# Performance work log

Measured on AMD Instinct MI355X. Metric: run time of the kernel, lower is better.

## Reference

```python
import jax, jax.numpy as jnp
import numpy as np

NUM_HEADS = 16
NEG_INF = -1e9


def setup_inputs() -> dict:
    key = jax.random.key(0)
    ks = jax.random.split(key, 12)
    T, B, E = 2048, 4, 1024
    s = 0.02
    inp = {
        "query": jax.random.normal(ks[0], (T, B, E), jnp.float32),
        "key": jax.random.normal(ks[1], (T, B, E), jnp.float32),
        "value": jax.random.normal(ks[2], (T, B, E), jnp.float32),
        # causal additive mask [T, S]: 0 on/below diagonal, -1e9 above
        "attn_mask": jnp.where(
            jnp.arange(T)[:, None] >= jnp.arange(T)[None, :], 0.0, NEG_INF
        ).astype(jnp.float32),
        "wq": jax.random.normal(ks[3], (E, E), jnp.float32) * s,
        "bq": jax.random.normal(ks[4], (E,), jnp.float32) * s,
        "wk": jax.random.normal(ks[5], (E, E), jnp.float32) * s,
        "bk": jax.random.normal(ks[6], (E,), jnp.float32) * s,
        "wv": jax.random.normal(ks[7], (E, E), jnp.float32) * s,
        "bv": jax.random.normal(ks[8], (E,), jnp.float32) * s,
        "wo": jax.random.normal(ks[9], (E, E), jnp.float32) * s,
        "bo": jax.random.normal(ks[10], (E,), jnp.float32) * s,
    }
    return inp


def reference(query, key, value, attn_mask, wq, bq, wk, bk, wv, bv, wo, bo):
    T, B, E = query.shape
    H = NUM_HEADS
    D = E // H
    scaling = D ** (-0.5)
    # projections (torch Linear: x @ W.T + b)
    q = (query @ wq.T + bq) * scaling          # [T, B, E]
    k = key @ wk.T + bk                         # [S, B, E]
    v = value @ wv.T + bv                       # [S, B, E]
    # -> [B*H, len, D]
    q = q.reshape(T, B * H, D).transpose(1, 0, 2)
    k = k.reshape(-1, B * H, D).transpose(1, 0, 2)
    v = v.reshape(-1, B * H, D).transpose(1, 0, 2)
    # scores [B*H, T, S], additive mask, softmax (dropout = identity in eval)
    attn_weights = jnp.einsum('ntd,nsd->nts', q, k) + attn_mask
    attn_weights = jax.nn.softmax(attn_weights, axis=-1)
    attn = jnp.einsum('nts,nsd->ntd', attn_weights, v)   # [B*H, T, D]
    attn = attn.transpose(1, 0, 2).reshape(T, B, E)
    return attn @ wo.T + bo
```

## Files before the change

### kernel.cpp

```cpp
#include <hip/hip_runtime.h>
#include <hip/hip_bf16.h>

typedef __hip_bfloat16 bf16;
typedef __attribute__((ext_vector_type(8))) short short8;
typedef __attribute__((ext_vector_type(4))) float float4v;
typedef __attribute__((ext_vector_type(2))) unsigned long long ull2;
typedef __attribute__((ext_vector_type(2))) unsigned int uint2v;

#define TLEN  2048
#define BATCH 4
#define EMB   1024
#define HEADS 16
#define HD    64
#define MROWS (TLEN*BATCH)
#define PSTRIDE 72
#define SMAX2 5.770780f
#define QSCALE 0.18033688f

#if __has_builtin(__builtin_amdgcn_exp2f)
#define EXP2(x) __builtin_amdgcn_exp2f(x)
#else
#define EXP2(x) exp2f(x)
#endif

__device__ __forceinline__ unsigned cvt_pk_bf16(float lo, float hi) {
    unsigned r;
    asm("v_cvt_pk_bf16_f32 %0, %1, %2" : "=v"(r) : "v"(lo), "v"(hi));
    return r;
}

__device__ __forceinline__ void gl2lds16(const bf16* g, bf16* l) {
    __builtin_amdgcn_global_load_lds(
        (const __attribute__((address_space(1))) void*)g,
        (__attribute__((address_space(3))) void*)l, 16, 0, 0);
}

__device__ __forceinline__ void store_out(float* p, float v)  { *p = v; }
__device__ __forceinline__ void store_out(bf16* p, float v)   { *p = __float2bfloat16(v); }

__device__ __forceinline__ void cvt8(const float* __restrict__ src,
                                     bf16* __restrict__ dst, int t) {
    const float4v a = ((const float4v*)src)[2*t];
    const float4v b = ((const float4v*)src)[2*t + 1];
    union { short8 v; bf16 h[8]; } u;
    u.h[0] = __float2bfloat16(a[0]);
    u.h[1] = __float2bfloat16(a[1]);
    u.h[2] = __float2bfloat16(a[2]);
    u.h[3] = __float2bfloat16(a[3]);
    u.h[4] = __float2bfloat16(b[0]);
    u.h[5] = __float2bfloat16(b[1]);
    u.h[6] = __float2bfloat16(b[2]);
    u.h[7] = __float2bfloat16(b[3]);
    ((short8*)dst)[t] = u.v;
}

__global__ __launch_bounds__(256)
void cvt_w(const float* __restrict__ wq, const float* __restrict__ wk,
           const float* __restrict__ wv, const float* __restrict__ wo,
           bf16* __restrict__ wqb, bf16* __restrict__ wkb,
           bf16* __restrict__ wvb, bf16* __restrict__ wob)
{
    const int id = blockIdx.x * 256 + threadIdx.x;
    const int NW = 1 << 17;
    const int w = id >> 17, off = id & (NW - 1);
    const float* s = w == 0 ? wq : (w == 1 ? wk : (w == 2 ? wv : wo));
    bf16*        d = w == 0 ? wqb : (w == 1 ? wkb : (w == 2 ? wvb : wob));
    cvt8(s, d, off);
}

template<int AMODE, typename OutT>
__device__ __forceinline__ void gemm_body(
    const void* __restrict__ Avp, const bf16* __restrict__ Bw,
    const float* __restrict__ bias, OutT* __restrict__ out,
    float scale, int mode, int bm, int bn)
{
    __shared__ __align__(16) bf16 smem[128*64*2];
    bf16* As = smem;
    bf16* Bs = smem + 128*64;
    const int tid  = threadIdx.x;
    const int lane = tid & 63;
    const int wave = tid >> 6;
    const int wm   = (wave >> 1) * 64;
    const int wn   = (wave & 1) * 64;
    const int quad = lane >> 4;
    const int l16  = lane & 15;
    const int hl   = wn >> 6;

    const int srow = tid >> 3;
    const int skc  = (tid & 7) ^ (srow & 7);
    const bf16*  Ag = nullptr;
    const float* Af = nullptr;
    if constexpr (AMODE == 0)
        Ag = (const bf16*)Avp + (size_t)(bm*128 + srow)*EMB + skc*8;
    else
        Af = (const float*)Avp + (size_t)(bm*128 + srow)*EMB + skc*8;
    const bf16* Bg = Bw + (size_t)(bn*128 + srow)*EMB + skc*8;
    bf16* Al = As + tid*8;
    bf16* Bl = Bs + tid*8;

    float4v acc[4][4];
    #pragma unroll
    for (int i=0;i<4;i++)
        #pragma unroll
        for (int j=0;j<4;j++) acc[i][j] = (float4v){0.f,0.f,0.f,0.f};

    for (int k0 = 0; k0 < EMB; k0 += 64) {
        float4v a0[4], a1[4];
        if constexpr (AMODE == 1) {
            #pragma unroll
            for (int g=0; g<4; g++) {
                const float* ap = Af + (size_t)g*32*EMB + k0;
                a0[g] = *(const float4v*)ap;
                a1[g] = *(const float4v*)(ap + 4);
            }
        }
        __syncthreads();
        #pragma unroll
        for (int g=0; g<4; g++)
            gl2lds16(Bg + (size_t)g*32*EMB + k0, Bl + g*2048);
        if constexpr (AMODE == 0) {
            #pragma unroll
            for (int g=0; g<4; g++)
                gl2lds16(Ag + (size_t)g*32*EMB + k0, Al + g*2048);
        } else {
            #pragma unroll
            for (int g=0; g<4; g++) {
                union { short8 v; unsigned u[4]; } p;
                p.u[0] = cvt_pk_bf16(a0[g][0], a0[g][1]);
                p.u[1] = cvt_pk_bf16(a0[g][2], a0[g][3]);
                p.u[2] = cvt_pk_bf16(a1[g][0], a1[g][1]);
                p.u[3] = cvt_pk_bf16(a1[g][2], a1[g][3]);
                *(short8*)(Al + g*2048) = p.v;
            }
        }
        __syncthreads();

        #pragma unroll
        for (int half=0; half<2; half++) {
            const int pc = (((half<<2) | quad) ^ (l16 & 7)) * 8;
            short8 af[4], bfr[4];
            #pragma unroll
            for (int i=0;i<4;i++)
                af[i] = *(const short8*)(As + (wm + i*16 + l16)*64 + pc);
            #pragma unroll
            for (int j=0;j<4;j++)
                bfr[j] = *(const short8*)(Bs + (wn + j*16 + l16)*64 + pc);
            #pragma unroll
            for (int i=0;i<4;i++)
                #pragma unroll
                for (int j=0;j<4;j++)
                    acc[i][j] = __builtin_amdgcn_mfma_f32_16x16x32_bf16(
                                    af[i], bfr[j], acc[i][j], 0, 0, 0);
        }
    }

    if (mode != 2) {
        #pragma unroll
        for (int i=0;i<4;i++) {
            #pragma unroll
            for (int j=0;j<4;j++) {
                const int n = bn*128 + wn + j*16 + l16;
                const float bf = bias[n];
                #pragma unroll
                for (int r=0;r<4;r++) {
                    const int m = bm*128 + wm + i*16 + quad*4 + r;
                    const float v = (acc[i][j][r] + bf) * scale;
                    size_t idx;
                    if (mode == 0) {
                        idx = (size_t)m*EMB + n;
                    } else {
                        const int t = m >> 2, b = m & 3;
                        const int h = n >> 6, d = n & 63;
                        idx = (((size_t)(b*HEADS + h))*TLEN + t)*HD + d;
                    }
                    store_out(out + idx, v);
                }
            }
        }
    } else {
        __syncthreads();
        bf16* Tb = smem;
        #pragma unroll
        for (int i=0;i<4;i++) {
            const int tc = (wm >> 4) + i;
            #pragma unroll
            for (int j=0;j<4;j++) {
                const int d = j*16 + l16;
                const float bf = bias[bn*128 + wn + d];
                #pragma unroll
                for (int r=0;r<4;r++) {
                    const float v = acc[i][j][r] + bf;
                    Tb[((((r<<1)|hl)*64 + d) << 5) + ((tc ^ (d & 7)) << 2) + quad]
                        = __float2bfloat16(v);
                }
            }
        }
        __syncthreads();
        bf16* ob = (bf16*)out;
        #pragma unroll
        for (int pass=0; pass<8; pass++) {
            const int row = pass*64 + (tid >> 2);
            const int c16 = tid & 3;
            const int b2  = row >> 7;
            const int h2l = (row >> 6) & 1;
            const int d   = row & 63;
            const int e   = d & 7;
            const unsigned long long lo =
                *(const unsigned long long*)(Tb + (row << 5) + ((( (2*c16)   ^ e) << 2)));
            const unsigned long long hi =
                *(const unsigned long long*)(Tb + (row << 5) + ((( (2*c16+1) ^ e) << 2)));
            ull2 val; val.x = lo; val.y = hi;
            *(ull2*)(ob + ((size_t)((b2*HEADS + bn*2 + h2l)*HD + d))*TLEN
                        + bm*32 + c16*8) = val;
        }
    }
}

__global__ __launch_bounds__(256, 2)
void gemm_qkv(const float* __restrict__ xq, const float* __restrict__ xk,
              const float* __restrict__ xv,
              const bf16* __restrict__ wq, const bf16* __restrict__ wk,
              const bf16* __restrict__ wv,
              const float* __restrict__ bq, const float* __restrict__ bk,
              const float* __restrict__ bv,
              bf16* __restrict__ oq, bf16* __restrict__ ok,
              bf16* __restrict__ ov)
{
    const int id  = blockIdx.x;
    const int xcd = id & 7;
    const int r   = id >> 3;
    const int z   = r >> 6;
    const int rem = r & 63;
    const int bm  = xcd + 8*(rem >> 3);
    const int bn  = rem & 7;

    const float* A  = z == 0 ? xq : (z == 1 ? xk : xv);
    const bf16*  W  = z == 0 ? wq : (z == 1 ? wk : wv);
    const float* bi = z == 0 ? bq : (z == 1 ? bk : bv);
    bf16*        o  = z == 0 ? oq : (z == 1 ? ok : ov);
    const float  sc = z == 0 ? QSCALE : 1.0f;
    const int    md = z == 2 ? 2 : 1;
    gemm_body<1, bf16>(A, W, bi, o, sc, md, bm, bn);
}

__global__ __launch_bounds__(256, 2)
void gemm_out(const bf16* __restrict__ A, const bf16* __restrict__ W,
              const float* __restrict__ bias, float* __restrict__ out)
{
    const int id  = blockIdx.x;
    const int xcd = id & 7;
    const int r   = id >> 3;
    const int bm  = xcd + 8*(r >> 3);
    const int bn  = r & 7;
    gemm_body<0, float>(A, W, bias, out, 1.0f, 0, bm, bn);
}

__global__ __launch_bounds__(256, 2)
void flash_attn(const bf16* __restrict__ Q, const bf16* __restrict__ K,
                const bf16* __restrict__ Vt, bf16* __restrict__ Aout)
{
    __shared__ __align__(16) bf16 Ks[2][64*64];
    __shared__ __align__(16) bf16 Vs[2][64*64];
    __shared__ __align__(16) bf16 Ps[4*32*PSTRIDE];
    const int tid  = threadIdx.x;
    const int lane = tid & 63;
    const int wave = tid >> 6;
    const int quad = lane >> 4;
    const int l16  = lane & 15;

    const int id  = blockIdx.x;
    const int xcd = id & 7;
    const int jj  = id >> 3;
    const int bh  = xcd + 8*(jj & 7);
    const int tq  = 15 - (jj >> 3);
    const int qbase = tq*128 + wave*32;

    short8 qf[2][2];
    #pragma unroll
    for (int f=0; f<2; f++) {
        const bf16* qrow = Q + ((size_t)bh*TLEN + qbase + f*16 + l16)*HD;
        qf[f][0] = *(const short8*)(qrow + quad*8);
        qf[f][1] = *(const short8*)(qrow + 32 + quad*8);
    }

    union { short8 v; short h[8]; } onesu;
    #pragma unroll
    for (int z=0; z<8; z++) onesu.h[z] = (short)0x3F80;
    const short8 ones8 = onesu.v;

    float4v o[2][4];
    float4v lsacc[2];
    #pragma unroll
    for (int f=0; f<2; f++) {
        lsacc[f] = (float4v){0.f,0.f,0.f,0.f};
        #pragma unroll
        for (int j=0;j<4;j++) { o[f][j] = (float4v){0.f,0.f,0.f,0.f}; }
    }

    bf16* Pw = Ps + wave*32*PSTRIDE;

    const int srow   = tid >> 3;
    const int schunk = (tid & 7) ^ (srow & 7);
    const bf16* Kg = K  + (size_t)bh*TLEN*HD + (size_t)srow*HD   + schunk*8;
    const bf16* Vg = Vt + (size_t)bh*HD*TLEN + (size_t)srow*TLEN + schunk*8;
    const int ldst = tid*8;

    const int nt = 2*tq + 2;
    gl2lds16(Kg,           &Ks[0][ldst]);
    gl2lds16(Kg + 32*HD,   &Ks[0][32*64 + ldst]);
    gl2lds16(Vg,           &Vs[0][ldst]);
    gl2lds16(Vg + 32*TLEN, &Vs[0][32*64 + ldst]);

    for (int i = 0; i < nt; i++) {
        const int buf = i & 1;
        __syncthreads();
        if (i + 1 < nt) {
            const int nb = buf ^ 1;
            const size_t s0n = (size_t)(i+1)*64;
            gl2lds16(Kg + s0n*HD,        &Ks[nb][ldst]);
            gl2lds16(Kg + (s0n+32)*HD,   &Ks[nb][32*64 + ldst]);
            gl2lds16(Vg + s0n,           &Vs[nb][ldst]);
            gl2lds16(Vg + 32*TLEN + s0n, &Vs[nb][32*64 + ldst]);
        }

        const bool live = (i*64) <= (qbase + 31);
        if (live) {

        float4v scr[2][4];
        #pragma unroll
        for (int f=0; f<2; f++)
            #pragma unroll
            for (int j=0;j<4;j++)
                scr[f][j] = (float4v){-SMAX2,-SMAX2,-SMAX2,-SMAX2};
        __builtin_amdgcn_s_setprio(1);
        #pragma unroll
        for (int h2=0; h2<2; h2++) {
            const int psw = ((h2<<2) | quad) ^ (l16 & 7);
            #pragma unroll
            for (int j=0;j<4;j++) {
                short8 kf = *(const short8*)(&Ks[buf][(j*16 + l16)*64 + psw*8]);
                scr[0][j] = __builtin_amdgcn_mfma_f32_16x16x32_bf16(kf, qf[0][h2], scr[0][j], 0,0,0);
                scr[1][j] = __builtin_amdgcn_mfma_f32_16x16x32_bf16(kf, qf[1][h2], scr[1][j], 0,0,0);
            }
        }
        __builtin_amdgcn_s_setprio(0);

        #pragma unroll
        for (int f=0; f<2; f++) {
            const int t = qbase + f*16 + l16;
            const bool needmask = (i*64 + 63) > (qbase + f*16);
            #pragma unroll
            for (int j=0;j<4;j++) {
                float p0, p1, p2, p3;
                if (needmask) {
                    const int s = i*64 + j*16 + quad*4;
                    p0 = (s   <= t) ? EXP2(scr[f][j][0]) : 0.f;
                    p1 = (s+1 <= t) ? EXP2(scr[f][j][1]) : 0.f;
                    p2 = (s+2 <= t) ? EXP2(scr[f][j][2]) : 0.f;
                    p3 = (s+3 <= t) ? EXP2(scr[f][j][3]) : 0.f;
                } else {
                    p0 = EXP2(scr[f][j][0]);
                    p1 = EXP2(scr[f][j][1]);
                    p2 = EXP2(scr[f][j][2]);
                    p3 = EXP2(scr[f][j][3]);
                }
                uint2v w;
                w.x = cvt_pk_bf16(p0, p1);
                w.y = cvt_pk_bf16(p2, p3);
                *(uint2v*)(Pw + (f*16 + l16)*PSTRIDE + j*16 + quad*4) = w;
            }
        }

        __builtin_amdgcn_s_setprio(1);
        #pragma unroll
        for (int h2=0; h2<2; h2++) {
            const int psw = ((h2<<2) | quad) ^ (l16 & 7);
            short8 pf0 = *(const short8*)(Pw + (l16)*PSTRIDE      + h2*32 + quad*8);
            short8 pf1 = *(const short8*)(Pw + (16 + l16)*PSTRIDE + h2*32 + quad*8);
            lsacc[0] = __builtin_amdgcn_mfma_f32_16x16x32_bf16(pf0, ones8, lsacc[0], 0,0,0);
            lsacc[1] = __builtin_amdgcn_mfma_f32_16x16x32_bf16(pf1, ones8, lsacc[1], 0,0,0);
            #pragma unroll
            for (int j=0;j<4;j++) {
                short8 vf = *(const short8*)(&Vs[buf][(j*16 + l16)*64 + psw*8]);
                o[0][j] = __builtin_amdgcn_mfma_f32_16x16x32_bf16(pf0, vf, o[0][j], 0,0,0);
                o[1][j] = __builtin_amdgcn_mfma_f32_16x16x32_bf16(pf1, vf, o[1][j], 0,0,0);
            }
        }
        __builtin_amdgcn_s_setprio(0);

        }
    }

    const int b = bh >> 4, h = bh & 15;
    #pragma unroll
    for (int f=0; f<2; f++) {
        float rn[4];
        #pragma unroll
        for (int r=0;r<4;r++)
            rn[r] = 1.0f / lsacc[f][r];
        #pragma unroll
        for (int j=0;j<4;j++)
            #pragma unroll
            for (int r=0;r<4;r++) {
                const int t = qbase + f*16 + quad*4 + r;
                const int d = j*16 + l16;
                Aout[((size_t)t*BATCH + b)*EMB + h*64 + d] =
                    __float2bfloat16(o[f][j][r] * rn[r]);
            }
    }
}

extern "C" void kernel_launch(void* const* d_in, const int* in_sizes, int n_in,
                              void* d_out, int out_size, void* d_ws, size_t ws_size,
                              hipStream_t stream)
{
    const float* query = (const float*)d_in[0];
    const float* key   = (const float*)d_in[1];
    const float* value = (const float*)d_in[2];
    const float* wq = (const float*)d_in[4];
    const float* bq = (const float*)d_in[5];
    const float* wk = (const float*)d_in[6];
    const float* bk = (const float*)d_in[7];
    const float* wv = (const float*)d_in[8];
    const float* bv = (const float*)d_in[9];
    const float* wo = (const float*)d_in[10];
    const float* bo = (const float*)d_in[11];

    const size_t actsz = (size_t)MROWS*EMB;
    const size_t wsz   = (size_t)EMB*EMB;
    bf16* wqb   = (bf16*)d_ws;
    bf16* wkb   = wqb + wsz;
    bf16* wvb   = wkb + wsz;
    bf16* wob   = wvb + wsz;
    bf16* q_ws  = wob + wsz;
    bf16* k_ws  = q_ws + actsz;
    bf16* v_ws  = k_ws + actsz;
    bf16* aout  = v_ws + actsz;

    const dim3 blk(256);

    hipLaunchKernelGGL(cvt_w, dim3(2048), blk, 0, stream,
                       wq, wk, wv, wo, wqb, wkb, wvb, wob);

    hipLaunchKernelGGL(gemm_qkv, dim3(1536), blk, 0, stream,
                       query, key, value, wqb, wkb, wvb, bq, bk, bv,
                       q_ws, k_ws, v_ws);

    hipLaunchKernelGGL(flash_attn, dim3(1024), blk, 0, stream,
                       q_ws, k_ws, v_ws, aout);

    hipLaunchKernelGGL(gemm_out, dim3(512), blk, 0, stream,
                       aout, wob, bo, (float*)d_out);
}
```

Before: 301.3 us.

## Double-buffer GEMM LDS tiles and prefetch next k-tile during MFMA

Restructures the projection GEMM main loop into a two-stage software pipeline: the next k-tile of A/B is issued to a second LDS buffer (or to registers for the fp32 A path) before computing on the current one. Explicit vmcnt/lgkmcnt waits and raw s_barrier replace the two __syncthreads per iteration. The aim is to hide global-load latency behind MFMA work. It uses more LDS (up to 64KB per block), which may cut occupancy, and relies on hand-counted waitcnt values being correct.

```diff
diff --git a/kernel.cpp b/kernel.cpp
--- a/kernel.cpp
+++ b/kernel.cpp
@@ -74,9 +74,7 @@
     const float* __restrict__ bias, OutT* __restrict__ out,
     float scale, int mode, int bm, int bn)
 {
-    __shared__ __align__(16) bf16 smem[128*64*2];
-    bf16* As = smem;
-    bf16* Bs = smem + 128*64;
+    __shared__ __align__(16) bf16 smem[(AMODE == 1 ? 3 : 4) * 128 * 64];
     const int tid  = threadIdx.x;
     const int lane = tid & 63;
     const int wave = tid >> 6;
@@ -95,8 +93,6 @@
     else
         Af = (const float*)Avp + (size_t)(bm*128 + srow)*EMB + skc*8;
     const bf16* Bg = Bw + (size_t)(bn*128 + srow)*EMB + skc*8;
-    bf16* Al = As + tid*8;
-    bf16* Bl = Bs + tid*8;
 
     float4v acc[4][4];
     #pragma unroll
@@ -104,53 +100,105 @@
         #pragma unroll
         for (int j=0;j<4;j++) acc[i][j] = (float4v){0.f,0.f,0.f,0.f};
 
-    for (int k0 = 0; k0 < EMB; k0 += 64) {
-        float4v a0[4], a1[4];
+    float4v aC[8], aN[8];
+
+    if constexpr (AMODE == 1) {
+        #pragma unroll
+        for (int g=0; g<4; g++) {
+            const float* ap = Af + (size_t)g*32*EMB;
+            aC[2*g]   = *(const float4v*)ap;
+            aC[2*g+1] = *(const float4v*)(ap + 4);
+        }
+        #pragma unroll
+        for (int g=0; g<4; g++)
+            gl2lds16(Bg + (size_t)g*32*EMB, smem + 8192 + tid*8 + g*2048);
+    } else {
+        #pragma unroll
+        for (int g=0; g<4; g++) {
+            gl2lds16(Ag + (size_t)g*32*EMB, smem + tid*8 + g*2048);
+            gl2lds16(Bg + (size_t)g*32*EMB, smem + 16384 + tid*8 + g*2048);
+        }
+    }
+
+    auto step = [&](int T, int sbA, int sbB, int sbAn, int sbBn,
+                    float4v (&aIn)[8], float4v (&aOut)[8]) {
+        const bool pf = (T + 1 < 16);
+        const int  k1 = (T + 1) * 64;
         if constexpr (AMODE == 1) {
+            asm volatile("s_waitcnt vmcnt(0)" ::: "memory");
+            __builtin_amdgcn_sched_barrier(0);
             #pragma unroll
             for (int g=0; g<4; g++) {
-                const float* ap = Af + (size_t)g*32*EMB + k0;
-                a0[g] = *(const float4v*)ap;
-                a1[g] = *(const float4v*)(ap + 4);
-            }
-        }
-        __syncthreads();
-        #pragma unroll
-        for (int g=0; g<4; g++)
-            gl2lds16(Bg + (size_t)g*32*EMB + k0, Bl + g*2048);
-        if constexpr (AMODE == 0) {
-            #pragma unroll
-            for (int g=0; g<4; g++)
-                gl2lds16(Ag + (size_t)g*32*EMB + k0, Al + g*2048);
+                union { short8 v; unsigned u[4]; } pk;
+                pk.u[0] = cvt_pk_bf16(aIn[2*g][0],   aIn[2*g][1]);
+                pk.u[1] = cvt_pk_bf16(aIn[2*g][2],   aIn[2*g][3]);
+                pk.u[2] = cvt_pk_bf16(aIn[2*g+1][0], aIn[2*g+1][1]);
+                pk.u[3] = cvt_pk_bf16(aIn[2*g+1][2], aIn[2*g+1][3]);
+                *(short8*)(smem + sbA + tid*8 + g*2048) = pk.v;
+            }
+            if (pf) {
+                #pragma unroll
+                for (int g=0; g<4; g++) {
+                    const float* ap = Af + (size_t)g*32*EMB + k1;
+                    aOut[2*g]   = *(const float4v*)ap;
+                    aOut[2*g+1] = *(const float4v*)(ap + 4);
+                }
+                #pragma unroll
+                for (int g=0; g<4; g++)
+                    gl2lds16(Bg + (size_t)g*32*EMB + k1,
+                             smem + sbBn + tid*8 + g*2048);
+            }
+            asm volatile("s_waitcnt lgkmcnt(0)" ::: "memory");
+            __builtin_amdgcn_sched_barrier(0);
+            __builtin_amdgcn_s_barrier();
+            asm volatile("" ::: "memory");
+            __builtin_amdgcn_sched_barrier(0);
         } else {
-            #pragma unroll
-            for (int g=0; g<4; g++) {
-                union { short8 v; unsigned u[4]; } p;
-                p.u[0] = cvt_pk_bf16(a0[g][0], a0[g][1]);
-                p.u[1] = cvt_pk_bf16(a0[g][2], a0[g][3]);
-                p.u[2] = cvt_pk_bf16(a1[g][0], a1[g][1]);
-                p.u[3] = cvt_pk_bf16(a1[g][2], a1[g][3]);
-                *(short8*)(Al + g*2048) = p.v;
-            }
-        }
-        __syncthreads();
-
+            if (pf) {
+                #pragma unroll
+                for (int g=0; g<4; g++) {
+                    gl2lds16(Ag + (size_t)g*32*EMB + k1, smem + sbAn + tid*8 + g*2048);
+                    gl2lds16(Bg + (size_t)g*32*EMB + k1, smem + sbBn + tid*8 + g*2048);
+                }
+                asm volatile("s_waitcnt vmcnt(8)" ::: "memory");
+            } else {
+                asm volatile("s_waitcnt vmcnt(0)" ::: "memory");
+            }
+            __builtin_amdgcn_sched_barrier(0);
+            __builtin_amdgcn_s_barrier();
+            asm volatile("" ::: "memory");
+            __builtin_amdgcn_sched_barrier(0);
+        }
         #pragma unroll
         for (int half=0; half<2; half++) {
             const int pc = (((half<<2) | quad) ^ (l16 & 7)) * 8;
-            short8 af[4], bfr[4];
-            #pragma unroll
-            for (int i=0;i<4;i++)
-                af[i] = *(const short8*)(As + (wm + i*16 + l16)*64 + pc);
-            #pragma unroll
-            for (int j=0;j<4;j++)
-                bfr[j] = *(const short8*)(Bs + (wn + j*16 + l16)*64 + pc);
-            #pragma unroll
-            for (int i=0;i<4;i++)
+            short8 af_[4], bf_[4];
+            #pragma unroll
+            for (int i2=0;i2<4;i2++)
+                af_[i2] = *(const short8*)(smem + sbA + (wm + i2*16 + l16)*64 + pc);
+            #pragma unroll
+            for (int j2=0;j2<4;j2++)
+                bf_[j2] = *(const short8*)(smem + sbB + (wn + j2*16 + l16)*64 + pc);
+            #pragma unroll
+            for (int i2=0;i2<4;i2++)
                 #pragma unroll
-                for (int j=0;j<4;j++)
-                    acc[i][j] = __builtin_amdgcn_mfma_f32_16x16x32_bf16(
-                                    af[i], bfr[j], acc[i][j], 0, 0, 0);
+                for (int j2=0;j2<4;j2++)
+                    acc[i2][j2] = __builtin_amdgcn_mfma_f32_16x16x32_bf16(
+                                      af_[i2], bf_[j2], acc[i2][j2], 0, 0, 0);
+        }
+        asm volatile("s_waitcnt lgkmcnt(0)" ::: "memory");
+        __builtin_amdgcn_sched_barrier(0);
+        __builtin_amdgcn_s_barrier();
+        asm volatile("" ::: "memory");
+    };
+
+    for (int tt = 0; tt < 16; tt += 2) {
+        if constexpr (AMODE == 1) {
+            step(tt,   0, 8192,  0, 16384, aC, aN);
+            step(tt+1, 0, 16384, 0, 8192,  aN, aC);
+        } else {
+            step(tt,   0,    16384, 8192, 24576, aC, aN);
+            step(tt+1, 8192, 24576, 0,    16384, aN, aC);
         }
     }
 
```

Result: slower. 321.2 us (+6.6%).
